# Kernel optimization log

Hardware: AMD Instinct MI355X
Metric: run time of the kernel (lower is better)

## Reference

```python
import jax, jax.numpy as jnp
import numpy as np

# Model dims: E experts, T total routed tokens, D model dim, H expert hidden dim
E, T, D, H = 8, 16384, 2048, 5632


def setup_inputs() -> dict:
    key = jax.random.key(0)
    k1, k2, k3, k4 = jax.random.split(key, 4)
    init_std = 0.02
    x = jax.random.normal(k1, (T, D), dtype=jnp.float32)
    # w1/w3: (num_experts, hidden_dim, dim); w2: (num_experts, dim, hidden_dim)
    w1 = jax.random.normal(k2, (E, H, D), dtype=jnp.float32) * init_std
    w2 = jax.random.normal(k3, (E, D, H), dtype=jnp.float32) * init_std
    w3 = jax.random.normal(k4, (E, H, D), dtype=jnp.float32) * init_std
    # Tokens are pre-sorted by expert; even split so sum == T (no padding path)
    num_tokens_per_expert = jnp.full((E,), T // E, dtype=jnp.int32)
    return {"x": x, "w1": w1, "w2": w2, "w3": w3,
            "num_tokens_per_expert": num_tokens_per_expert}


def reference(x, w1, w2, w3, num_tokens_per_expert):
    """Grouped-GEMM SwiGLU experts: out[t] = silu(x@w1[e].T) * (x@w3[e].T) @ w2[e].T
    where e is the expert owning token t (tokens sorted by expert).
    lax.ragged_dot is the exact grouped-GEMM primitive: lhs (m,k), rhs (g,k,n),
    group_sizes (g,) -> (m,n). Weights are stored as (g, out, in), so swap to (g, in, out),
    matching the torch matmul with transpose(-2, -1).
    """
    groups = num_tokens_per_expert.astype(jnp.int32)
    gate = jax.lax.ragged_dot(x, jnp.swapaxes(w1, 1, 2), groups)   # (T, H)
    up = jax.lax.ragged_dot(x, jnp.swapaxes(w3, 1, 2), groups)     # (T, H)
    h = jax.nn.silu(gate) * up                                      # fused SwiGLU
    out = jax.lax.ragged_dot(h, jnp.swapaxes(w2, 1, 2), groups)    # (T, D)
    return out
```

## Files before the change

kernel.cpp:

```cpp
#include <hip/hip_runtime.h>
#include <hip/hip_bf16.h>


typedef __bf16 bf16x8 __attribute__((ext_vector_type(8)));
typedef float f32x4 __attribute__((ext_vector_type(4)));
typedef unsigned short u16x8 __attribute__((ext_vector_type(8)));

constexpr int E = 8;
constexpr int T = 16384;
constexpr int D = 2048;
constexpr int H = 5632;

#define DEV static __device__ __forceinline__

DEV unsigned short f2bf(float f) {
    unsigned u = __builtin_bit_cast(unsigned, f);
    u = (u + 0x7FFFu + ((u >> 16) & 1u)) >> 16;
    return (unsigned short)u;
}

DEV void gload16(const void* g, void* l) {
    __builtin_amdgcn_global_load_lds(
        (const __attribute__((address_space(1))) void*)g,
        (__attribute__((address_space(3))) void*)l, 16, 0, 0);
}

DEV f32x4 mfma16(bf16x8 a, bf16x8 b, f32x4 c) {
    return __builtin_amdgcn_mfma_f32_16x16x32_bf16(a, b, c, 0, 0, 0);
}

DEV void cvt8(const float* src, unsigned short* dst) {
    float4 a = *(const float4*)src;
    float4 c = *(const float4*)(src + 4);
    u16x8 r;
    r[0] = f2bf(a.x); r[1] = f2bf(a.y); r[2] = f2bf(a.z); r[3] = f2bf(a.w);
    r[4] = f2bf(c.x); r[5] = f2bf(c.y); r[6] = f2bf(c.z); r[7] = f2bf(c.w);
    *(u16x8*)dst = r;
}

__global__ __launch_bounds__(256) void k_cvt_pre(
    const float* __restrict__ x, const float* __restrict__ w1,
    const float* __restrict__ w3, unsigned short* __restrict__ xb,
    unsigned short* __restrict__ w13b) {
    const int bid = blockIdx.x, tid = threadIdx.x;
    if (bid < 512) {
        const long n8 = (long)T * D / 8;
        for (long i = (long)bid * 256 + tid; i < n8; i += 512L * 256)
            cvt8(x + i * 8, xb + i * 8);
    } else {
        const int which = (bid < 1280) ? 0 : 1;
        const float* src = which ? w3 : w1;
        const long b0 = which ? 1280 : 512;
        const long n8 = (long)E * H * D / 8;
        for (long i = ((long)bid - b0) * 256 + tid; i < n8; i += 768L * 256) {
            int col8 = (int)(i & 255);
            int rowi = (int)(i >> 8);
            int e = rowi / H;
            int h = rowi - e * H;
            int rr = ((h >> 4) << 5) + (which << 4) + (h & 15);
            cvt8(src + i * 8,
                 w13b + ((size_t)e * (2 * H) + rr) * D + (size_t)col8 * 8);
        }
    }
}

__global__ __launch_bounds__(256) void k_cvt(const float* __restrict__ in,
                                             unsigned short* __restrict__ out,
                                             long n8) {
    long i = (long)blockIdx.x * blockDim.x + threadIdx.x;
    long stride = (long)gridDim.x * blockDim.x;
    for (; i < n8; i += stride) cvt8(in + i * 8, out + i * 8);
}

DEV int expert_of_row(const int* __restrict__ ntp, int row0) {
    int e = 0, s = 0;
    for (int i = 0; i < E; ++i) {
        int c = ntp[i];
        if (row0 < s + c) { e = i; break; }
        s += c;
    }
    return e;
}

template <int LD, int NT>
DEV void gemm_4p2(const unsigned short* pa, const unsigned short* pb,
                  unsigned short* sA, unsigned short* sB, int tid,
                  f32x4 (&acc)[8][4]) {
    const int lane = tid & 63, wid = tid >> 6;
    const int wm = wid >> 2, wn = wid & 3;

    const int q8 = (((lane >> 4) ^ ((lane >> 1) & 3)) << 3);
    const int aoff = (wm * 128 + (lane & 15)) * 32 + q8;
    const int boff = (wn * 64 + (lane & 15)) * 32 + q8;

    char* lA = (char*)sA;
    char* lB = (char*)sB;
    const int dW = wid << 10;

    auto stA = [&](int t, int kk) {
        const unsigned short* g = pa + (size_t)t * 64 + kk * 32;
        char* l = lA + ((t & 1) << 15) + (kk << 14) + dW;
        gload16(g, l);
        gload16(g + (size_t)128 * LD, l + 8192);
    };
    auto stB = [&](int t, int kk) {
        const unsigned short* g = pb + (size_t)t * 64 + kk * 32;
        char* l = lB + ((t & 1) << 15) + (kk << 14) + dW;
        gload16(g, l);
        gload16(g + (size_t)128 * LD, l + 8192);
    };

    stA(0, 0); stB(0, 0); stA(0, 1); stB(0, 1);
    asm volatile("s_waitcnt vmcnt(4)" ::: "memory");
    __builtin_amdgcn_s_barrier();
    __builtin_amdgcn_sched_barrier(0);

#pragma unroll 1
    for (int t = 0; t < NT; ++t) {
        const int sb = (t & 1) << 14;
        const unsigned short* A0 = sA + sb + aoff;
        const unsigned short* B0 = sB + sb + boff;
        const unsigned short* A1 = A0 + 8192;
        const unsigned short* B1 = B0 + 8192;
        const bool more = (t + 1 < NT);
        bf16x8 a[4], b[4];

#pragma unroll
        for (int i = 0; i < 4; ++i) a[i] = *(const bf16x8*)(A0 + i * 512);
#pragma unroll
        for (int i = 0; i < 4; ++i) b[i] = *(const bf16x8*)(B0 + i * 512);
        if (more) stA(t + 1, 0);
        __builtin_amdgcn_s_setprio(1);
#pragma unroll
        for (int m = 0; m < 4; ++m)
#pragma unroll
            for (int n = 0; n < 4; ++n)
                acc[m][n] = mfma16(a[m], b[n], acc[m][n]);
        __builtin_amdgcn_s_setprio(0);

#pragma unroll
        for (int i = 0; i < 4; ++i)
            a[i] = *(const bf16x8*)(A0 + 2048 + i * 512);
        if (more) stB(t + 1, 0);
        __builtin_amdgcn_s_setprio(1);
#pragma unroll
        for (int m = 0; m < 4; ++m)
#pragma unroll
            for (int n = 0; n < 4; ++n)
                acc[4 + m][n] = mfma16(a[m], b[n], acc[4 + m][n]);
        __builtin_amdgcn_s_setprio(0);

        if (more) asm volatile("s_waitcnt vmcnt(4)" ::: "memory");
        else      asm volatile("s_waitcnt vmcnt(0)" ::: "memory");
        __builtin_amdgcn_s_barrier();
        __builtin_amdgcn_sched_barrier(0);

#pragma unroll
        for (int i = 0; i < 4; ++i) a[i] = *(const bf16x8*)(A1 + i * 512);
#pragma unroll
        for (int i = 0; i < 4; ++i) b[i] = *(const bf16x8*)(B1 + i * 512);
        if (more) stA(t + 1, 1);
        __builtin_amdgcn_s_setprio(1);
#pragma unroll
        for (int m = 0; m < 4; ++m)
#pragma unroll
            for (int n = 0; n < 4; ++n)
                acc[m][n] = mfma16(a[m], b[n], acc[m][n]);
        __builtin_amdgcn_s_setprio(0);

#pragma unroll
        for (int i = 0; i < 4; ++i)
            a[i] = *(const bf16x8*)(A1 + 2048 + i * 512);
        if (more) stB(t + 1, 1);
        __builtin_amdgcn_s_setprio(1);
#pragma unroll
        for (int m = 0; m < 4; ++m)
#pragma unroll
            for (int n = 0; n < 4; ++n)
                acc[4 + m][n] = mfma16(a[m], b[n], acc[4 + m][n]);
        __builtin_amdgcn_s_setprio(0);

        if (more) {
            asm volatile("s_waitcnt vmcnt(4)" ::: "memory");
            __builtin_amdgcn_s_barrier();
            __builtin_amdgcn_sched_barrier(0);
        }
    }
}

__global__ __launch_bounds__(512, 2) void k_gate_up(
    const unsigned short* __restrict__ xb,
    const unsigned short* __restrict__ w13b,
    const float* __restrict__ w2, unsigned short* __restrict__ w2b,
    const int* __restrict__ ntp, unsigned short* __restrict__ hbuf) {
    __shared__ unsigned short sA[2 * 2 * 8192];
    __shared__ unsigned short sB[2 * 2 * 8192];

    const int bid = blockIdx.x;
    const int tid = threadIdx.x;

    if (w2) {
        const float* src = w2 + (size_t)bid * 32768;
        unsigned short* dst = w2b + (size_t)bid * 32768;
#pragma unroll
        for (int it = 0; it < 8; ++it) {
            int o = (it * 512 + tid) * 8;
            cvt8(src + o, dst + o);
        }
        asm volatile("s_waitcnt vmcnt(0)" ::: "memory");
    }

    const int tm = (bid & 7) * 8 + ((bid >> 3) & 7);
    const int tn = bid >> 6;

    const int row0 = tm << 8;
    const int e = expert_of_row(ntp, row0);
    const int lane = tid & 63, wid = tid >> 6;

    const int sr = tid >> 2;
    const int sq = (tid & 3) ^ ((tid >> 3) & 3);
    const unsigned short* pa = xb + (size_t)(row0 + sr) * D + sq * 8;
    const unsigned short* pb = w13b + (size_t)e * (2 * H) * D +
                               (size_t)((tn << 8) + sr) * D + sq * 8;

    f32x4 acc[8][4] = {};
    gemm_4p2<D, D / 64>(pa, pb, sA, sB, tid, acc);

    const int wm = wid >> 2, wn = wid & 3;
    const int rbase = row0 + (wm << 7) + ((lane >> 4) << 2);
    const int cb = (((tn << 3) + (wn << 1)) << 4) + (lane & 15);
#pragma unroll
    for (int mi = 0; mi < 8; ++mi)
#pragma unroll
        for (int pi = 0; pi < 2; ++pi) {
            f32x4 g = acc[mi][2 * pi], u = acc[mi][2 * pi + 1];
            const int hcol = cb + (pi << 4);
#pragma unroll
            for (int j = 0; j < 4; ++j) {
                float gv = g[j];
                float hv = gv * u[j] / (1.f + __expf(-gv));
                hbuf[(size_t)(rbase + (mi << 4) + j) * H + hcol] = f2bf(hv);
            }
        }
}

__global__ __launch_bounds__(512, 2) void k_down(
    const unsigned short* __restrict__ hbuf,
    const unsigned short* __restrict__ w2b,
    const int* __restrict__ ntp,
    float* __restrict__ out) {
    __shared__ unsigned short sA[2 * 2 * 8192];
    __shared__ unsigned short sB[2 * 2 * 8192];

    const int bid = blockIdx.x;
    const int xcd = bid & 7;
    const int j = bid >> 3;
    const int tn = j & 7;
    const int tm = xcd * 8 + (j >> 3);

    const int row0 = tm << 8;
    const int e = expert_of_row(ntp, row0);
    const int tid = threadIdx.x;
    const int lane = tid & 63, wid = tid >> 6;

    const int sr = tid >> 2;
    const int sq = (tid & 3) ^ ((tid >> 3) & 3);
    const unsigned short* pa = hbuf + (size_t)(row0 + sr) * H + sq * 8;
    const unsigned short* pb = w2b + (size_t)e * D * H +
                               (size_t)((tn << 8) + sr) * H + sq * 8;

    f32x4 acc[8][4] = {};
    gemm_4p2<H, H / 64>(pa, pb, sA, sB, tid, acc);

    const int wm = wid >> 2, wn = wid & 3;
    const int rbase = row0 + (wm << 7) + ((lane >> 4) << 2);
    const int cb = (tn << 8) + (wn << 6) + (lane & 15);
#pragma unroll
    for (int mi = 0; mi < 8; ++mi)
#pragma unroll
        for (int ni = 0; ni < 4; ++ni) {
            f32x4 c = acc[mi][ni];
#pragma unroll
            for (int j2 = 0; j2 < 4; ++j2)
                out[(size_t)(rbase + (mi << 4) + j2) * D + cb + (ni << 4)] =
                    c[j2];
        }
}

extern "C" void kernel_launch(void* const* d_in, const int* in_sizes, int n_in,
                              void* d_out, int out_size, void* d_ws,
                              size_t ws_size, hipStream_t stream) {
    const float* x = (const float*)d_in[0];
    const float* w1 = (const float*)d_in[1];
    const float* w2 = (const float*)d_in[2];
    const float* w3 = (const float*)d_in[3];
    const int* ntp = (const int*)d_in[4];
    float* out = (float*)d_out;

    char* ws = (char*)d_ws;
    unsigned short* xb = (unsigned short*)(ws + 0);
    unsigned short* w13b = (unsigned short*)(ws + 67108864L);
    unsigned short* hbuf = (unsigned short*)(ws + 436207616L);
    const bool big = ws_size >= 805306368UL;
    unsigned short* w2b = big ? (unsigned short*)(ws + 620756992L) : w13b;

    k_cvt_pre<<<2048, 256, 0, stream>>>(x, w1, w3, xb, w13b);

    k_gate_up<<<(T / 256) * (2 * H / 256), 512, 0, stream>>>(
        xb, w13b, big ? w2 : nullptr, big ? w2b : nullptr, ntp, hbuf);

    if (!big)
        k_cvt<<<2048, 256, 0, stream>>>(w2, w2b, (long)E * D * H / 8);

    k_down<<<(T / 256) * (D / 256), 512, 0, stream>>>(hbuf, w2b, ntp, out);
}
```

Measured before the change: 1.353 ms.

## Load A operand directly from global into registers, bypassing LDS

The A tile is no longer staged through shared memory. Each lane loads its MFMA A fragments straight from global memory into registers, double-buffered across k-halves, while B keeps the LDS double buffer. This halves LDS use and the LDS read traffic for A. In exchange, A rows are loaded redundantly by the four waves that share a wm, which raises global/L2 traffic. It also adds register pressure from 16 bf16x8 A fragments and uses uncoalesced 16-byte strided loads, which could hurt occupancy and latency hiding.

```diff
diff --git a/kernel.cpp b/kernel.cpp
--- a/kernel.cpp
+++ b/kernel.cpp
@@ -83,26 +83,18 @@
 }
 
 template <int LD, int NT>
-DEV void gemm_4p2(const unsigned short* pa, const unsigned short* pb,
-                  unsigned short* sA, unsigned short* sB, int tid,
-                  f32x4 (&acc)[8][4]) {
+DEV void gemm_ad(const unsigned short* __restrict__ pa_lane,
+                 const unsigned short* __restrict__ pb,
+                 unsigned short* sB, int tid, f32x4 (&acc)[8][4]) {
     const int lane = tid & 63, wid = tid >> 6;
-    const int wm = wid >> 2, wn = wid & 3;
+    const int wn = wid & 3;
 
     const int q8 = (((lane >> 4) ^ ((lane >> 1) & 3)) << 3);
-    const int aoff = (wm * 128 + (lane & 15)) * 32 + q8;
     const int boff = (wn * 64 + (lane & 15)) * 32 + q8;
 
-    char* lA = (char*)sA;
     char* lB = (char*)sB;
     const int dW = wid << 10;
 
-    auto stA = [&](int t, int kk) {
-        const unsigned short* g = pa + (size_t)t * 64 + kk * 32;
-        char* l = lA + ((t & 1) << 15) + (kk << 14) + dW;
-        gload16(g, l);
-        gload16(g + (size_t)128 * LD, l + 8192);
-    };
     auto stB = [&](int t, int kk) {
         const unsigned short* g = pb + (size_t)t * 64 + kk * 32;
         char* l = lB + ((t & 1) << 15) + (kk << 14) + dW;
@@ -110,78 +102,62 @@
         gload16(g + (size_t)128 * LD, l + 8192);
     };
 
-    stA(0, 0); stB(0, 0); stA(0, 1); stB(0, 1);
-    asm volatile("s_waitcnt vmcnt(4)" ::: "memory");
+    bf16x8 aX[8], aY[8], b[4];
+
+    auto loadA = [&](bf16x8 (&dst)[8], int t, int kk) {
+        const unsigned short* g = pa_lane + (size_t)t * 64 + kk * 32;
+#pragma unroll
+        for (int m = 0; m < 8; ++m)
+            dst[m] = *(const bf16x8*)(g + (size_t)m * 16 * LD);
+    };
+
+    stB(0, 0); stB(0, 1);
+    __builtin_amdgcn_sched_barrier(0);
+    loadA(aX, 0, 0);
+    asm volatile("s_waitcnt vmcnt(8)" ::: "memory");
     __builtin_amdgcn_s_barrier();
     __builtin_amdgcn_sched_barrier(0);
 
 #pragma unroll 1
     for (int t = 0; t < NT; ++t) {
         const int sb = (t & 1) << 14;
-        const unsigned short* A0 = sA + sb + aoff;
         const unsigned short* B0 = sB + sb + boff;
-        const unsigned short* A1 = A0 + 8192;
         const unsigned short* B1 = B0 + 8192;
         const bool more = (t + 1 < NT);
-        bf16x8 a[4], b[4];
-
-#pragma unroll
-        for (int i = 0; i < 4; ++i) a[i] = *(const bf16x8*)(A0 + i * 512);
+
 #pragma unroll
         for (int i = 0; i < 4; ++i) b[i] = *(const bf16x8*)(B0 + i * 512);
-        if (more) stA(t + 1, 0);
+        if (more) stB(t + 1, 0);
+        loadA(aY, t, 1);
         __builtin_amdgcn_s_setprio(1);
 #pragma unroll
-        for (int m = 0; m < 4; ++m)
+        for (int m = 0; m < 8; ++m)
 #pragma unroll
             for (int n = 0; n < 4; ++n)
-                acc[m][n] = mfma16(a[m], b[n], acc[m][n]);
+                acc[m][n] = mfma16(aX[m], b[n], acc[m][n]);
         __builtin_amdgcn_s_setprio(0);
 
-#pragma unroll
-        for (int i = 0; i < 4; ++i)
-            a[i] = *(const bf16x8*)(A0 + 2048 + i * 512);
-        if (more) stB(t + 1, 0);
-        __builtin_amdgcn_s_setprio(1);
-#pragma unroll
-        for (int m = 0; m < 4; ++m)
-#pragma unroll
-            for (int n = 0; n < 4; ++n)
-                acc[4 + m][n] = mfma16(a[m], b[n], acc[4 + m][n]);
-        __builtin_amdgcn_s_setprio(0);
-
-        if (more) asm volatile("s_waitcnt vmcnt(4)" ::: "memory");
-        else      asm volatile("s_waitcnt vmcnt(0)" ::: "memory");
+        if (more) asm volatile("s_waitcnt vmcnt(10)" ::: "memory");
+        else      asm volatile("s_waitcnt vmcnt(8)" ::: "memory");
         __builtin_amdgcn_s_barrier();
         __builtin_amdgcn_sched_barrier(0);
 
 #pragma unroll
-        for (int i = 0; i < 4; ++i) a[i] = *(const bf16x8*)(A1 + i * 512);
-#pragma unroll
         for (int i = 0; i < 4; ++i) b[i] = *(const bf16x8*)(B1 + i * 512);
-        if (more) stA(t + 1, 1);
+        if (more) {
+            stB(t + 1, 1);
+            loadA(aX, t + 1, 0);
+        }
         __builtin_amdgcn_s_setprio(1);
 #pragma unroll
-        for (int m = 0; m < 4; ++m)
+        for (int m = 0; m < 8; ++m)
 #pragma unroll
             for (int n = 0; n < 4; ++n)
-                acc[m][n] = mfma16(a[m], b[n], acc[m][n]);
+                acc[m][n] = mfma16(aY[m], b[n], acc[m][n]);
         __builtin_amdgcn_s_setprio(0);
 
-#pragma unroll
-        for (int i = 0; i < 4; ++i)
-            a[i] = *(const bf16x8*)(A1 + 2048 + i * 512);
-        if (more) stB(t + 1, 1);
-        __builtin_amdgcn_s_setprio(1);
-#pragma unroll
-        for (int m = 0; m < 4; ++m)
-#pragma unroll
-            for (int n = 0; n < 4; ++n)
-                acc[4 + m][n] = mfma16(a[m], b[n], acc[4 + m][n]);
-        __builtin_amdgcn_s_setprio(0);
-
         if (more) {
-            asm volatile("s_waitcnt vmcnt(4)" ::: "memory");
+            asm volatile("s_waitcnt vmcnt(10)" ::: "memory");
             __builtin_amdgcn_s_barrier();
             __builtin_amdgcn_sched_barrier(0);
         }
@@ -193,7 +169,6 @@
     const unsigned short* __restrict__ w13b,
     const float* __restrict__ w2, unsigned short* __restrict__ w2b,
     const int* __restrict__ ntp, unsigned short* __restrict__ hbuf) {
-    __shared__ unsigned short sA[2 * 2 * 8192];
     __shared__ unsigned short sB[2 * 2 * 8192];
 
     const int bid = blockIdx.x;
@@ -216,17 +191,18 @@
     const int row0 = tm << 8;
     const int e = expert_of_row(ntp, row0);
     const int lane = tid & 63, wid = tid >> 6;
-
+    const int wm = wid >> 2, wn = wid & 3;
+
+    const unsigned short* pa_lane =
+        xb + (size_t)(row0 + wm * 128 + (lane & 15)) * D + ((lane >> 4) << 3);
     const int sr = tid >> 2;
     const int sq = (tid & 3) ^ ((tid >> 3) & 3);
-    const unsigned short* pa = xb + (size_t)(row0 + sr) * D + sq * 8;
     const unsigned short* pb = w13b + (size_t)e * (2 * H) * D +
                                (size_t)((tn << 8) + sr) * D + sq * 8;
 
     f32x4 acc[8][4] = {};
-    gemm_4p2<D, D / 64>(pa, pb, sA, sB, tid, acc);
-
-    const int wm = wid >> 2, wn = wid & 3;
+    gemm_ad<D, D / 64>(pa_lane, pb, sB, tid, acc);
+
     const int rbase = row0 + (wm << 7) + ((lane >> 4) << 2);
     const int cb = (((tn << 3) + (wn << 1)) << 4) + (lane & 15);
 #pragma unroll
@@ -249,7 +225,6 @@
     const unsigned short* __restrict__ w2b,
     const int* __restrict__ ntp,
     float* __restrict__ out) {
-    __shared__ unsigned short sA[2 * 2 * 8192];
     __shared__ unsigned short sB[2 * 2 * 8192];
 
     const int bid = blockIdx.x;
@@ -262,17 +237,19 @@
     const int e = expert_of_row(ntp, row0);
     const int tid = threadIdx.x;
     const int lane = tid & 63, wid = tid >> 6;
-
+    const int wm = wid >> 2, wn = wid & 3;
+
+    const unsigned short* pa_lane =
+        hbuf + (size_t)(row0 + wm * 128 + (lane & 15)) * H +
+        ((lane >> 4) << 3);
     const int sr = tid >> 2;
     const int sq = (tid & 3) ^ ((tid >> 3) & 3);
-    const unsigned short* pa = hbuf + (size_t)(row0 + sr) * H + sq * 8;
     const unsigned short* pb = w2b + (size_t)e * D * H +
                                (size_t)((tn << 8) + sr) * H + sq * 8;
 
     f32x4 acc[8][4] = {};
-    gemm_4p2<H, H / 64>(pa, pb, sA, sB, tid, acc);
-
-    const int wm = wid >> 2, wn = wid & 3;
+    gemm_ad<H, H / 64>(pa_lane, pb, sB, tid, acc);
+
     const int rbase = row0 + (wm << 7) + ((lane >> 4) << 2);
     const int cb = (tn << 8) + (wn << 6) + (lane & 15);
 #pragma unroll
```

Result: slower. 2.771 ms (+104.8%).
